# Optimization experiments

Measured on AMD Instinct MI355X. Metric: run time of the kernel, lower is better.

Reference implementation:

```python
import jax, jax.numpy as jnp
import numpy as np


def setup_inputs() -> dict:
    key = jax.random.key(0)
    k1, k2 = jax.random.split(key)
    B, C, H, W = 2, 1, 64, 64
    HW = H * W
    pred = jax.random.uniform(k1, (B, C, H, W), dtype=jnp.float32)
    token = jax.random.uniform(k2, (B, HW, HW), dtype=jnp.float32)
    return {"pred": pred, "token": token}


def reference(pred, token):
    # pred: [B, 1, H, W] -> p: [B, HW]
    B = pred.shape[0]
    p = pred.reshape(B, -1)
    q = 1.0 - p
    # sum(f_token)  = sum_bij p_bi * token_bij
    # sum(fore_A)   = sum_bij p_bi * token_bij * p_bj  (bilinear quadratic form)
    # sum(b_token)  = sum_bij (1-p_bi) * token_bij
    # sum(back_B)   = sum_bij (1-p_bi) * token_bij * (1-p_bj)
    s_f = jnp.einsum('bi,bij->', p, token)
    s_fa = jnp.einsum('bi,bij,bj->', p, token, p)
    s_b = jnp.einsum('bi,bij->', q, token)
    s_bb = jnp.einsum('bi,bij,bj->', q, token, q)
    gsa_loss = 2.0 - s_fa / s_f - s_bb / s_b
    return gsa_loss
```

## Files before the change

### kernel.cpp

```cpp
#include <hip/hip_runtime.h>


#define HW   4096
#define HW4  1024
#define NBLK 512
#define RPW  4

struct alignas(32) D4 { double t, f, c, fa; };

__global__ __launch_bounds__(256, 2) void gsa_partial(
    const float* __restrict__ pred,
    const float* __restrict__ token,
    D4* __restrict__ part)
{
    __shared__ float4 pj_lds[HW4];
    __shared__ double sm[4][4];

    const float4* __restrict__ tok4  = (const float4*)token;
    const float4* __restrict__ pred4 = (const float4*)pred;

    const int bid  = blockIdx.x;
    const int wave = threadIdx.x >> 6;
    const int lane = threadIdx.x & 63;
    const int gw   = bid * 4 + wave;
    const int row0 = gw * RPW;
    const int b    = row0 >> 12;

    for (int k = threadIdx.x; k < HW4; k += 256)
        pj_lds[k] = pred4[b * HW4 + k];

    float pi_r[RPW];
#pragma unroll
    for (int r = 0; r < RPW; ++r)
        pi_r[r] = pred[row0 + r];

    float4 A[16], Bv[16];
    {
        const float4* __restrict__ rp = tok4 + (size_t)row0 * HW4;
#pragma unroll
        for (int u = 0; u < 16; ++u)
            A[u] = rp[u * 64 + lane];
    }

    __syncthreads();

    float tT = 0.f, tF = 0.f, tC = 0.f, tFA = 0.f;

#pragma unroll
    for (int r = 0; r < RPW; ++r) {
        float4* cur = (r & 1) ? Bv : A;
        float4* nxt = (r & 1) ? A  : Bv;

        if (r + 1 < RPW) {
            const float4* __restrict__ rp = tok4 + (size_t)(row0 + r + 1) * HW4;
#pragma unroll
            for (int u = 0; u < 16; ++u)
                nxt[u] = rp[u * 64 + lane];
        }
        __builtin_amdgcn_sched_barrier(0);

        float s0 = 0.f, s1 = 0.f, d0 = 0.f, d1 = 0.f;
#pragma unroll
        for (int u = 0; u < 16; u += 2) {
            float4 pa = pj_lds[u * 64 + lane];
            float4 pb = pj_lds[(u + 1) * 64 + lane];
            s0 += cur[u].x + cur[u].y + cur[u].z + cur[u].w;
            d0 += cur[u].x * pa.x + cur[u].y * pa.y + cur[u].z * pa.z + cur[u].w * pa.w;
            s1 += cur[u+1].x + cur[u+1].y + cur[u+1].z + cur[u+1].w;
            d1 += cur[u+1].x * pb.x + cur[u+1].y * pb.y + cur[u+1].z * pb.z + cur[u+1].w * pb.w;
        }
        float s = s0 + s1, d = d0 + d1;
        float pi = pi_r[r];
        tT  += s;
        tF  += pi * s;
        tC  += d;
        tFA += pi * d;
    }

    for (int off = 32; off > 0; off >>= 1) {
        tT  += __shfl_down(tT,  off);
        tF  += __shfl_down(tF,  off);
        tC  += __shfl_down(tC,  off);
        tFA += __shfl_down(tFA, off);
    }

    if (lane == 0) {
        sm[wave][0] = (double)tT;
        sm[wave][1] = (double)tF;
        sm[wave][2] = (double)tC;
        sm[wave][3] = (double)tFA;
    }
    __syncthreads();

    if (threadIdx.x == 0) {
        D4 p;
        p.t  = sm[0][0] + sm[1][0] + sm[2][0] + sm[3][0];
        p.f  = sm[0][1] + sm[1][1] + sm[2][1] + sm[3][1];
        p.c  = sm[0][2] + sm[1][2] + sm[2][2] + sm[3][2];
        p.fa = sm[0][3] + sm[1][3] + sm[2][3] + sm[3][3];
        part[bid] = p;
    }
}

__global__ __launch_bounds__(256) void gsa_final(
    const D4* __restrict__ part, float* __restrict__ out)
{
    const double2* __restrict__ p2 = (const double2*)part;

    double aT = 0.0, aF = 0.0, aC = 0.0, aFA = 0.0;
    for (int k = threadIdx.x; k < NBLK; k += 256) {
        double2 lo = p2[k * 2 + 0];
        double2 hi = p2[k * 2 + 1];
        aT += lo.x; aF += lo.y; aC += hi.x; aFA += hi.y;
    }

    for (int off = 32; off > 0; off >>= 1) {
        aT  += __shfl_down(aT,  off);
        aF  += __shfl_down(aF,  off);
        aC  += __shfl_down(aC,  off);
        aFA += __shfl_down(aFA, off);
    }

    __shared__ double sm[4][4];
    const int wave = threadIdx.x >> 6;
    const int lane = threadIdx.x & 63;
    if (lane == 0) {
        sm[wave][0] = aT; sm[wave][1] = aF;
        sm[wave][2] = aC; sm[wave][3] = aFA;
    }
    __syncthreads();

    if (threadIdx.x == 0) {
        double T   = sm[0][0] + sm[1][0] + sm[2][0] + sm[3][0];
        double sf  = sm[0][1] + sm[1][1] + sm[2][1] + sm[3][1];
        double sc  = sm[0][2] + sm[1][2] + sm[2][2] + sm[3][2];
        double sfa = sm[0][3] + sm[1][3] + sm[2][3] + sm[3][3];
        double sb  = T - sf;
        double sbb = T - sf - sc + sfa;
        out[0] = (float)(2.0 - sfa / sf - sbb / sb);
    }
}

extern "C" void kernel_launch(void* const* d_in, const int* in_sizes, int n_in,
                              void* d_out, int out_size, void* d_ws, size_t ws_size,
                              hipStream_t stream)
{
    const float* pred  = (const float*)d_in[0];
    const float* token = (const float*)d_in[1];
    float* out  = (float*)d_out;
    D4*    part = (D4*)d_ws;

    gsa_partial<<<NBLK, 256, 0, stream>>>(pred, token, part);
    gsa_final<<<1, 256, 0, stream>>>(part, out);
}
```

Before: 30.09 us.

## Fuse final reduction into partial kernel via last-block atomic counter

Merges the two kernels into one: each block writes its partial sums with agent-scope atomic stores, then bumps a hierarchical counter (8 groups of 64 blocks plus a root counter). The last block to finish does the global reduction and writes the loss. This removes the second kernel launch and its gap, but adds a memset of the counters before each launch, plus atomics and fences at the end of every block.

```diff
diff --git a/kernel.cpp b/kernel.cpp
--- a/kernel.cpp
+++ b/kernel.cpp
@@ -1,20 +1,27 @@
 #include <hip/hip_runtime.h>
 
 
-#define HW   4096
-#define HW4  1024
-#define NBLK 512
-#define RPW  4
+#define HW    4096
+#define HW4   1024
+#define NBLK  512
+#define RPW   4
+#define NGRP  8
 
 struct alignas(32) D4 { double t, f, c, fa; };
 
-__global__ __launch_bounds__(256, 2) void gsa_partial(
+#define CTR_OFF   16384
+#define CTR_BYTES (64 * (NGRP + 1))
+
+__global__ __launch_bounds__(256, 2) void gsa_fused(
     const float* __restrict__ pred,
     const float* __restrict__ token,
-    D4* __restrict__ part)
+    double* __restrict__ partd,
+    unsigned* __restrict__ ctr,
+    float* __restrict__ out)
 {
     __shared__ float4 pj_lds[HW4];
     __shared__ double sm[4][4];
+    __shared__ int    last_flag;
 
     const float4* __restrict__ tok4  = (const float4*)token;
     const float4* __restrict__ pred4 = (const float4*)pred;
@@ -93,25 +100,35 @@
     __syncthreads();
 
     if (threadIdx.x == 0) {
-        D4 p;
-        p.t  = sm[0][0] + sm[1][0] + sm[2][0] + sm[3][0];
-        p.f  = sm[0][1] + sm[1][1] + sm[2][1] + sm[3][1];
-        p.c  = sm[0][2] + sm[1][2] + sm[2][2] + sm[3][2];
-        p.fa = sm[0][3] + sm[1][3] + sm[2][3] + sm[3][3];
-        part[bid] = p;
+        double pt  = sm[0][0] + sm[1][0] + sm[2][0] + sm[3][0];
+        double pf  = sm[0][1] + sm[1][1] + sm[2][1] + sm[3][1];
+        double pc  = sm[0][2] + sm[1][2] + sm[2][2] + sm[3][2];
+        double pfa = sm[0][3] + sm[1][3] + sm[2][3] + sm[3][3];
+        __hip_atomic_store(&partd[bid*4+0], pt,  __ATOMIC_RELAXED, __HIP_MEMORY_SCOPE_AGENT);
+        __hip_atomic_store(&partd[bid*4+1], pf,  __ATOMIC_RELAXED, __HIP_MEMORY_SCOPE_AGENT);
+        __hip_atomic_store(&partd[bid*4+2], pc,  __ATOMIC_RELAXED, __HIP_MEMORY_SCOPE_AGENT);
+        __hip_atomic_store(&partd[bid*4+3], pfa, __ATOMIC_RELAXED, __HIP_MEMORY_SCOPE_AGENT);
+        __threadfence();
+
+        int lst = 0;
+        unsigned t = atomicAdd(&ctr[(bid >> 6) * 16], 1u);
+        if (t == 63u) {
+            unsigned rt = atomicAdd(&ctr[NGRP * 16], 1u);
+            lst = (rt == NGRP - 1u);
+        }
+        last_flag = lst;
     }
-}
+    __syncthreads();
 
-__global__ __launch_bounds__(256) void gsa_final(
-    const D4* __restrict__ part, float* __restrict__ out)
-{
-    const double2* __restrict__ p2 = (const double2*)part;
+    if (!last_flag) return;
 
+    __threadfence();
     double aT = 0.0, aF = 0.0, aC = 0.0, aFA = 0.0;
     for (int k = threadIdx.x; k < NBLK; k += 256) {
-        double2 lo = p2[k * 2 + 0];
-        double2 hi = p2[k * 2 + 1];
-        aT += lo.x; aF += lo.y; aC += hi.x; aFA += hi.y;
+        aT  += __hip_atomic_load(&partd[k*4+0], __ATOMIC_RELAXED, __HIP_MEMORY_SCOPE_AGENT);
+        aF  += __hip_atomic_load(&partd[k*4+1], __ATOMIC_RELAXED, __HIP_MEMORY_SCOPE_AGENT);
+        aC  += __hip_atomic_load(&partd[k*4+2], __ATOMIC_RELAXED, __HIP_MEMORY_SCOPE_AGENT);
+        aFA += __hip_atomic_load(&partd[k*4+3], __ATOMIC_RELAXED, __HIP_MEMORY_SCOPE_AGENT);
     }
 
     for (int off = 32; off > 0; off >>= 1) {
@@ -121,9 +138,7 @@
         aFA += __shfl_down(aFA, off);
     }
 
-    __shared__ double sm[4][4];
-    const int wave = threadIdx.x >> 6;
-    const int lane = threadIdx.x & 63;
+    __syncthreads();
     if (lane == 0) {
         sm[wave][0] = aT; sm[wave][1] = aF;
         sm[wave][2] = aC; sm[wave][3] = aFA;
@@ -147,9 +162,11 @@
 {
     const float* pred  = (const float*)d_in[0];
     const float* token = (const float*)d_in[1];
-    float* out  = (float*)d_out;
-    D4*    part = (D4*)d_ws;
+    float*    out   = (float*)d_out;
+    double*   partd = (double*)d_ws;
+    unsigned* ctr   = (unsigned*)((char*)d_ws + CTR_OFF);
 
-    gsa_partial<<<NBLK, 256, 0, stream>>>(pred, token, part);
-    gsa_final<<<1, 256, 0, stream>>>(part, out);
+    hipMemsetAsync((char*)d_ws + CTR_OFF, 0, CTR_BYTES, stream);
+
+    gsa_fused<<<NBLK, 256, 0, stream>>>(pred, token, partd, ctr, out);
 }
```

Measured after the change: 45.89 us. +52.5%, slower.
